# Kernel optimization log

Measured on AMD Instinct MI355X. Metric: run time of the kernel, lower is better.

Reference implementation:

```python
import jax, jax.numpy as jnp
import numpy as np

N_NODES = 50000
N_EDGES = 1600000
IN_FEAT = 128
HEADS = 8
OUT_FEAT = 16


def setup_inputs() -> dict:
    key = jax.random.key(0)
    ks = jax.random.split(key, 8)
    feat = jax.random.normal(ks[0], (N_NODES, IN_FEAT), dtype=jnp.float32)
    src = jax.random.randint(ks[1], (N_EDGES,), 0, N_NODES, dtype=jnp.int32)
    dst = jax.random.randint(ks[2], (N_EDGES,), 0, N_NODES, dtype=jnp.int32)
    eps = jax.random.normal(ks[3], (N_EDGES, HEADS), dtype=jnp.float32)
    # small init scale keeps exp(log_scale) numerically tame
    W_fc = jax.random.normal(ks[4], (IN_FEAT, HEADS * OUT_FEAT), dtype=jnp.float32) * 0.05
    W_post = jax.random.normal(ks[5], (OUT_FEAT, 4), dtype=jnp.float32) * 0.05
    b_post = jax.random.normal(ks[6], (4,), dtype=jnp.float32) * 0.05
    bias = jax.random.normal(ks[7], (HEADS, OUT_FEAT), dtype=jnp.float32) * 0.05
    return {"feat": feat, "src": src, "dst": dst, "eps": eps,
            "W_fc": W_fc, "W_post": W_post, "b_post": b_post, "bias": bias}


def reference(feat, src, dst, eps, W_fc, W_post, b_post, bias):
    N = feat.shape[0]
    # node projection: [N, H, F]
    h = (feat @ W_fc).reshape(N, HEADS, OUT_FEAT)
    # per-node posterior params: [N, H, 4] -> loc_l, loc_r, log_scale_l, log_scale_r
    post = jnp.einsum('nhf,fk->nhk', h, W_post) + b_post
    loc_l, loc_r, lsl, lsr = post[..., 0], post[..., 1], post[..., 2], post[..., 3]
    # per-edge score via reparameterized sample: [E, H]
    loc = loc_l[src] + loc_r[dst]
    log_scale = lsl[src] + lsr[dst]
    e = loc + jnp.exp(log_scale) * eps
    # edge softmax over incoming edges of each dst node (per head)
    m = jax.lax.stop_gradient(jax.ops.segment_max(e, dst, num_segments=N))
    ex = jnp.exp(e - m[dst])
    denom = jax.ops.segment_sum(ex, dst, num_segments=N)
    a = ex / denom[dst]
    # weighted aggregation: sum over in-edges of h[src] * a
    msg = h[src] * a[:, :, None]                     # [E, H, F]
    out = jax.ops.segment_sum(msg, dst, num_segments=N)  # [N, H, F]
    out = out + bias[None]
    return out
```

## Files before the change

### kernel.cpp

```cpp
#include <hip/hip_runtime.h>
#include <hip/hip_fp16.h>

#define IN_FEAT 128
#define HEADS 8
#define OUT_FEAT 16
#define HF 128
#define BSHIFT 6
#define BNODES 64
#define NBMAX 1024
#define CHUNK 4096
#define CAP 2560

__global__ __launch_bounds__(256) void init_kernel(int* __restrict__ bucket_cursor,
                                                   int nb)
{
    int i = blockIdx.x * 256 + threadIdx.x;
    if (i < nb) bucket_cursor[i] = i * CAP;
}

__device__ __forceinline__ void gemm_body(
    const float* __restrict__ feat, const float* __restrict__ W_fc,
    const float* __restrict__ W_post, const float* __restrict__ b_post,
    __half* __restrict__ hbuf, float2* __restrict__ postE,
    float2* __restrict__ postD, int N, int node_base, void* ldsraw)
{
    float4* lds4 = (float4*)ldsraw;
    float* lds = (float*)lds4;
    const int tid = threadIdx.x;

    const float4* f4 = (const float4*)feat;
    for (int i = tid; i < 32 * 32; i += 256) {
        int n = i >> 5, k4 = i & 31;
        int gn = node_base + n;
        float4 v = make_float4(0.f, 0.f, 0.f, 0.f);
        if (gn < N) v = f4[gn * 32 + k4];
        lds4[i] = v;
    }
    __syncthreads();

    const int cg = tid & 31, ng = tid >> 5;
    const int n0 = ng * 4;
    float acc[4][4];
#pragma unroll
    for (int i = 0; i < 4; i++) acc[i][0] = acc[i][1] = acc[i][2] = acc[i][3] = 0.f;

    const float4* W4 = (const float4*)W_fc;
#pragma unroll 4
    for (int k = 0; k < 128; ++k) {
        float4 w = W4[k * 32 + cg];
#pragma unroll
        for (int i = 0; i < 4; i++) {
            float f = lds[(n0 + i) * 128 + k];
            acc[i][0] += f * w.x; acc[i][1] += f * w.y;
            acc[i][2] += f * w.z; acc[i][3] += f * w.w;
        }
    }
    __half2* hb2 = (__half2*)hbuf;
#pragma unroll
    for (int i = 0; i < 4; i++) {
        int gn = node_base + n0 + i;
        if (gn < N) {
            union { uint2 u; __half2 h[2]; } pk;
            pk.h[0] = __floats2half2_rn(acc[i][0], acc[i][1]);
            pk.h[1] = __floats2half2_rn(acc[i][2], acc[i][3]);
            *(uint2*)&hb2[gn * 64 + cg * 2] = pk.u;
        }
    }
    __syncthreads();
#pragma unroll
    for (int i = 0; i < 4; i++)
        lds4[(n0 + i) * 32 + cg] = make_float4(acc[i][0], acc[i][1], acc[i][2], acc[i][3]);
    __syncthreads();

    {
        int n = tid >> 3, h = tid & 7;
        float p0 = b_post[0], p1 = b_post[1], p2 = b_post[2], p3 = b_post[3];
#pragma unroll
        for (int f = 0; f < 16; ++f) {
            float v = lds[n * 128 + h * 16 + f];
            p0 += v * W_post[f * 4 + 0];
            p1 += v * W_post[f * 4 + 1];
            p2 += v * W_post[f * 4 + 2];
            p3 += v * W_post[f * 4 + 3];
        }
        int gn = node_base + n;
        if (gn < N) {
            postE[gn * 8 + h] = make_float2(p0, p2);
            postD[gn * 8 + h] = make_float2(p1, p3);
        }
    }
}

__global__ __launch_bounds__(256) void gemm_scatter_kernel(
    const float* __restrict__ feat, const float* __restrict__ W_fc,
    const float* __restrict__ W_post, const float* __restrict__ b_post,
    __half* __restrict__ hbuf, float2* __restrict__ postE,
    float2* __restrict__ postD, int N,
    const int* __restrict__ src, const int* __restrict__ dst,
    int* __restrict__ bucket_cursor, uint2* __restrict__ recs, int E, int nb,
    int SB)
{
    __shared__ float4 lds4[32 * 32];
    const int tid = threadIdx.x;

    if (blockIdx.x < SB) {
        int* cnt  = (int*)lds4;
        int* base = cnt + NBMAX;
        for (int i = tid; i < nb; i += 256) cnt[i] = 0;
        __syncthreads();
        const int e0 = blockIdx.x * CHUNK;
        const int e1 = min(e0 + CHUNK, E);
        for (int e = e0 + tid; e < e1; e += 256)
            atomicAdd(&cnt[dst[e] >> BSHIFT], 1);
        __syncthreads();
        for (int i = tid; i < nb; i += 256) {
            int c = cnt[i];
            base[i] = c ? atomicAdd(&bucket_cursor[i], c) : 0;
            cnt[i] = 0;
        }
        __syncthreads();
        for (int e = e0 + tid; e < e1; e += 256) {
            int d = dst[e];
            int b = d >> BSHIFT;
            int slot = base[b] + atomicAdd(&cnt[b], 1);
            if (slot < (b + 1) * CAP)
                recs[slot] = make_uint2((unsigned)e,
                                        ((unsigned)src[e] << BSHIFT) | (unsigned)(d & (BNODES - 1)));
        }
        return;
    }

    gemm_body(feat, W_fc, W_post, b_post, hbuf, postE, postD, N,
              (int)(blockIdx.x - SB) * 32, (void*)lds4);
}

__global__ __launch_bounds__(256) void bucket_csr_kernel(
    const uint2* __restrict__ recs, const int* __restrict__ bucket_cursor,
    uint2* __restrict__ offs, uint2* __restrict__ csr, int N)
{
    __shared__ int ncnt[BNODES];
    __shared__ int snc[BNODES];
    const int b = blockIdx.x, tid = threadIdx.x;
    const int node_lo = b << BSHIFT;
    const int rlo = b * CAP;
    int rhi = bucket_cursor[b];
    if (rhi > rlo + CAP) rhi = rlo + CAP;
    const int gn = node_lo + tid;

    if (tid < BNODES) ncnt[tid] = 0;
    __syncthreads();
    for (int r = rlo + tid; r < rhi; r += 256)
        atomicAdd(&ncnt[recs[r].y & (BNODES - 1u)], 1);
    __syncthreads();
    if (tid < BNODES) snc[tid] = ncnt[tid];
    __syncthreads();
    for (int off = 1; off < BNODES; off <<= 1) {
        int t = (tid < BNODES && tid >= off) ? snc[tid - off] : 0;
        __syncthreads();
        if (tid < BNODES) snc[tid] += t;
        __syncthreads();
    }
    int cnt = (tid < BNODES) ? ncnt[tid] : 0;
    int excl = (tid < BNODES) ? snc[tid] - cnt : 0;
    if (tid < BNODES && gn < N) offs[gn] = make_uint2(rlo + excl, cnt);
    __syncthreads();
    if (tid < BNODES) ncnt[tid] = excl;
    __syncthreads();

    for (int r = rlo + tid; r < rhi; r += 256) {
        uint2 rec = recs[r];
        int dl = (int)(rec.y & (BNODES - 1u));
        unsigned s = rec.y >> BSHIFT;
        int slot = rlo + atomicAdd(&ncnt[dl], 1);
        csr[slot] = make_uint2(rec.x, s);
    }
}

__global__ __launch_bounds__(256) void agg_kernel(
    const uint2* __restrict__ csr, const uint2* __restrict__ offs,
    const float2* __restrict__ postE, const float2* __restrict__ postD,
    const float* __restrict__ eps,
    const __half* __restrict__ hbuf, const float* __restrict__ bias,
    float* __restrict__ out, int N)
{
    const int lane = threadIdx.x & 63;
    const int d = blockIdx.x * 4 + (threadIdx.x >> 6);
    if (d >= N) return;
    const uint2 od = offs[d];
    const int start = (int)od.x;
    const int deg = (int)od.y;
    const int j = lane >> 3, hh = lane & 7;
    const float2 dv = postD[(size_t)d * 8 + hh];

    float2 acc = make_float2(0.f, 0.f);
    float dsum = 0.f;

    int c = 0;
    for (; c + 8 <= deg; c += 8) {
        uint2 rec = csr[start + c + j];
        int e = (int)rec.x, s = (int)rec.y;
        float2 pv = postE[(size_t)s * 8 + hh];
        float ep = eps[(size_t)e * 8 + hh];
        float ex = __expf((pv.x + dv.x) + __expf(pv.y + dv.y) * ep);
#pragma unroll
        for (int jj = 0; jj < 8; ++jj) {
            float a = __shfl(ex, jj * 8 + j, 64);
            int  sj = __shfl(s, jj * 8, 64);
            float2 hv = __half22float2(((const __half2*)(hbuf + (size_t)sj * HF))[lane]);
            acc.x += a * hv.x;
            acc.y += a * hv.y;
            dsum += a;
        }
    }
    if (c < deg) {
        int jc = deg - c;
        uint2 rec = csr[start + c + min(j, jc - 1)];
        int e = (int)rec.x, s = (int)rec.y;
        float2 pv = postE[(size_t)s * 8 + hh];
        float ep = eps[(size_t)e * 8 + hh];
        float ex = (j < jc) ? __expf((pv.x + dv.x) + __expf(pv.y + dv.y) * ep) : 0.f;
        for (int jj = 0; jj < jc; ++jj) {
            float a = __shfl(ex, jj * 8 + j, 64);
            int  sj = __shfl(s, jj * 8, 64);
            float2 hv = __half22float2(((const __half2*)(hbuf + (size_t)sj * HF))[lane]);
            acc.x += a * hv.x;
            acc.y += a * hv.y;
            dsum += a;
        }
    }

    float inv = (dsum > 0.f) ? 1.f / dsum : 0.f;
    float2 bv = ((const float2*)bias)[lane];
    float2 o = make_float2(acc.x * inv + bv.x, acc.y * inv + bv.y);
    ((float2*)out)[(size_t)d * 64 + lane] = o;
}

extern "C" void kernel_launch(void* const* d_in, const int* in_sizes, int n_in,
                              void* d_out, int out_size, void* d_ws, size_t ws_size,
                              hipStream_t stream)
{
    const float* feat   = (const float*)d_in[0];
    const int*   src    = (const int*)d_in[1];
    const int*   dst    = (const int*)d_in[2];
    const float* eps    = (const float*)d_in[3];
    const float* W_fc   = (const float*)d_in[4];
    const float* W_post = (const float*)d_in[5];
    const float* b_post = (const float*)d_in[6];
    const float* bias   = (const float*)d_in[7];
    float* out = (float*)d_out;

    const int N = in_sizes[0] / IN_FEAT;
    const int E = in_sizes[1];
    const int nb = (N + BNODES - 1) >> BSHIFT;
    const int SB = (E + CHUNK - 1) / CHUNK;
    const int GB = (N + 31) / 32;

    char* p = (char*)d_ws;
    auto alloc = [&](size_t bytes) {
        char* r = p;
        p += (bytes + 255) & ~size_t(255);
        return r;
    };
    __half* hbuf    = (__half*)alloc((size_t)N * HF * 2);
    float2* postE   = (float2*)alloc((size_t)N * 8 * 8);
    float2* postD   = (float2*)alloc((size_t)N * 8 * 8);
    uint2*  offs    = (uint2*)alloc((size_t)N * 8);
    int*    bucket_cursor = (int*)alloc((size_t)(NBMAX + 1) * 4);
    uint2*  recs    = (uint2*)alloc((size_t)nb * CAP * 8);
    uint2*  csr     = (uint2*)alloc((size_t)nb * CAP * 8);

    init_kernel<<<(nb + 255) / 256, 256, 0, stream>>>(bucket_cursor, nb);
    gemm_scatter_kernel<<<SB + GB, 256, 0, stream>>>(
        feat, W_fc, W_post, b_post, hbuf, postE, postD, N,
        src, dst, bucket_cursor, recs, E, nb, SB);
    bucket_csr_kernel<<<nb, 256, 0, stream>>>(recs, bucket_cursor, offs, csr, N);
    agg_kernel<<<(N + 3) / 4, 256, 0, stream>>>(csr, offs, postE, postD, eps,
                                                hbuf, bias, out, N);
}
```

Measured before the change: 292.3 us.

## Pack eps to fp16 into bucket records and use 16-bit permutation instead of CSR copy

The scatter phase now reads each edge's eps row, converts it to half precision and stores it next to the bucketed record, so the aggregation reads eps from bucket-local memory rather than gathering randomly from the full fp32 eps array. The second pass writes only a 16-bit permutation index per edge instead of copying full CSR records. The aggregation kernel loads up to 64 permutation entries per wave and resolves src and eps through them. This trades random 32-byte eps gathers and a record copy for an extra indirection, half-precision eps (reduced accuracy), and larger scatter writes.

```diff
diff --git a/kernel.cpp b/kernel.cpp
--- a/kernel.cpp
+++ b/kernel.cpp
@@ -97,8 +97,9 @@
     __half* __restrict__ hbuf, float2* __restrict__ postE,
     float2* __restrict__ postD, int N,
     const int* __restrict__ src, const int* __restrict__ dst,
-    int* __restrict__ bucket_cursor, uint2* __restrict__ recs, int E, int nb,
-    int SB)
+    const float* __restrict__ eps,
+    int* __restrict__ bucket_cursor, unsigned* __restrict__ recsA,
+    uint4* __restrict__ recsE, int E, int nb, int SB)
 {
     __shared__ float4 lds4[32 * 32];
     const int tid = threadIdx.x;
@@ -119,13 +120,22 @@
             cnt[i] = 0;
         }
         __syncthreads();
+        const float4* e4 = (const float4*)eps;
         for (int e = e0 + tid; e < e1; e += 256) {
             int d = dst[e];
             int b = d >> BSHIFT;
             int slot = base[b] + atomicAdd(&cnt[b], 1);
-            if (slot < (b + 1) * CAP)
-                recs[slot] = make_uint2((unsigned)e,
-                                        ((unsigned)src[e] << BSHIFT) | (unsigned)(d & (BNODES - 1)));
+            if (slot < (b + 1) * CAP) {
+                float4 lo = e4[(size_t)e * 2];
+                float4 hi = e4[(size_t)e * 2 + 1];
+                union { uint4 u; __half2 h[4]; } pk;
+                pk.h[0] = __floats2half2_rn(lo.x, lo.y);
+                pk.h[1] = __floats2half2_rn(lo.z, lo.w);
+                pk.h[2] = __floats2half2_rn(hi.x, hi.y);
+                pk.h[3] = __floats2half2_rn(hi.z, hi.w);
+                recsA[slot] = ((unsigned)src[e] << BSHIFT) | (unsigned)(d & (BNODES - 1));
+                recsE[slot] = pk.u;
+            }
         }
         return;
     }
@@ -134,9 +144,9 @@
               (int)(blockIdx.x - SB) * 32, (void*)lds4);
 }
 
-__global__ __launch_bounds__(256) void bucket_csr_kernel(
-    const uint2* __restrict__ recs, const int* __restrict__ bucket_cursor,
-    uint2* __restrict__ offs, uint2* __restrict__ csr, int N)
+__global__ __launch_bounds__(256) void perm_kernel(
+    const unsigned* __restrict__ recsA, const int* __restrict__ bucket_cursor,
+    unsigned short* __restrict__ perm16, uint2* __restrict__ offs, int N)
 {
     __shared__ int ncnt[BNODES];
     __shared__ int snc[BNODES];
@@ -150,7 +160,7 @@
     if (tid < BNODES) ncnt[tid] = 0;
     __syncthreads();
     for (int r = rlo + tid; r < rhi; r += 256)
-        atomicAdd(&ncnt[recs[r].y & (BNODES - 1u)], 1);
+        atomicAdd(&ncnt[recsA[r] & (BNODES - 1u)], 1);
     __syncthreads();
     if (tid < BNODES) snc[tid] = ncnt[tid];
     __syncthreads();
@@ -168,18 +178,16 @@
     __syncthreads();
 
     for (int r = rlo + tid; r < rhi; r += 256) {
-        uint2 rec = recs[r];
-        int dl = (int)(rec.y & (BNODES - 1u));
-        unsigned s = rec.y >> BSHIFT;
-        int slot = rlo + atomicAdd(&ncnt[dl], 1);
-        csr[slot] = make_uint2(rec.x, s);
+        int dl = (int)(recsA[r] & (BNODES - 1u));
+        int q = atomicAdd(&ncnt[dl], 1);
+        perm16[rlo + q] = (unsigned short)(r - rlo);
     }
 }
 
 __global__ __launch_bounds__(256) void agg_kernel(
-    const uint2* __restrict__ csr, const uint2* __restrict__ offs,
+    const unsigned* __restrict__ recsA, const uint4* __restrict__ recsE,
+    const unsigned short* __restrict__ perm16, const uint2* __restrict__ offs,
     const float2* __restrict__ postE, const float2* __restrict__ postD,
-    const float* __restrict__ eps,
     const __half* __restrict__ hbuf, const float* __restrict__ bias,
     float* __restrict__ out, int N)
 {
@@ -189,44 +197,56 @@
     const uint2 od = offs[d];
     const int start = (int)od.x;
     const int deg = (int)od.y;
+    const int rbase = (d >> BSHIFT) * CAP;
     const int j = lane >> 3, hh = lane & 7;
     const float2 dv = postD[(size_t)d * 8 + hh];
+    const __half* epsH = (const __half*)recsE;
 
     float2 acc = make_float2(0.f, 0.f);
     float dsum = 0.f;
 
     int c = 0;
-    for (; c + 8 <= deg; c += 8) {
-        uint2 rec = csr[start + c + j];
-        int e = (int)rec.x, s = (int)rec.y;
-        float2 pv = postE[(size_t)s * 8 + hh];
-        float ep = eps[(size_t)e * 8 + hh];
-        float ex = __expf((pv.x + dv.x) + __expf(pv.y + dv.y) * ep);
-#pragma unroll
-        for (int jj = 0; jj < 8; ++jj) {
-            float a = __shfl(ex, jj * 8 + j, 64);
-            int  sj = __shfl(s, jj * 8, 64);
-            float2 hv = __half22float2(((const __half2*)(hbuf + (size_t)sj * HF))[lane]);
-            acc.x += a * hv.x;
-            acc.y += a * hv.y;
-            dsum += a;
-        }
-    }
-    if (c < deg) {
-        int jc = deg - c;
-        uint2 rec = csr[start + c + min(j, jc - 1)];
-        int e = (int)rec.x, s = (int)rec.y;
-        float2 pv = postE[(size_t)s * 8 + hh];
-        float ep = eps[(size_t)e * 8 + hh];
-        float ex = (j < jc) ? __expf((pv.x + dv.x) + __expf(pv.y + dv.y) * ep) : 0.f;
-        for (int jj = 0; jj < jc; ++jj) {
-            float a = __shfl(ex, jj * 8 + j, 64);
-            int  sj = __shfl(s, jj * 8, 64);
-            float2 hv = __half22float2(((const __half2*)(hbuf + (size_t)sj * HF))[lane]);
-            acc.x += a * hv.x;
-            acc.y += a * hv.y;
-            dsum += a;
-        }
+    while (c < deg) {
+        const int win = min(64, deg - c);
+        int li = c + ((lane < win) ? lane : (win - 1));
+        int p_all = (int)perm16[start + li];
+        int s_all = (int)(recsA[rbase + p_all] >> BSHIFT);
+
+        int cw = 0;
+        for (; cw + 8 <= win; cw += 8) {
+            int pj = __shfl(p_all, cw + j, 64);
+            int sj = __shfl(s_all, cw + j, 64);
+            float ep = __half2float(epsH[(size_t)(rbase + pj) * 8 + hh]);
+            float2 pv = postE[(size_t)sj * 8 + hh];
+            float ex = __expf((pv.x + dv.x) + __expf(pv.y + dv.y) * ep);
+#pragma unroll
+            for (int jj = 0; jj < 8; ++jj) {
+                float a = __shfl(ex, jj * 8 + j, 64);
+                int  sg = __shfl(s_all, cw + jj, 64);
+                float2 hv = __half22float2(((const __half2*)(hbuf + (size_t)sg * HF))[lane]);
+                acc.x += a * hv.x;
+                acc.y += a * hv.y;
+                dsum += a;
+            }
+        }
+        if (cw < win) {
+            int jc = win - cw;
+            int jj0 = cw + ((j < jc) ? j : (jc - 1));
+            int pj = __shfl(p_all, jj0, 64);
+            int sj = __shfl(s_all, jj0, 64);
+            float ep = __half2float(epsH[(size_t)(rbase + pj) * 8 + hh]);
+            float2 pv = postE[(size_t)sj * 8 + hh];
+            float ex = (j < jc) ? __expf((pv.x + dv.x) + __expf(pv.y + dv.y) * ep) : 0.f;
+            for (int jj = 0; jj < jc; ++jj) {
+                float a = __shfl(ex, jj * 8 + j, 64);
+                int  sg = __shfl(s_all, cw + jj, 64);
+                float2 hv = __half22float2(((const __half2*)(hbuf + (size_t)sg * HF))[lane]);
+                acc.x += a * hv.x;
+                acc.y += a * hv.y;
+                dsum += a;
+            }
+        }
+        c += win;
     }
 
     float inv = (dsum > 0.f) ? 1.f / dsum : 0.f;
@@ -266,14 +286,15 @@
     float2* postD   = (float2*)alloc((size_t)N * 8 * 8);
     uint2*  offs    = (uint2*)alloc((size_t)N * 8);
     int*    bucket_cursor = (int*)alloc((size_t)(NBMAX + 1) * 4);
-    uint2*  recs    = (uint2*)alloc((size_t)nb * CAP * 8);
-    uint2*  csr     = (uint2*)alloc((size_t)nb * CAP * 8);
+    unsigned*       recsA = (unsigned*)alloc((size_t)nb * CAP * 4);
+    uint4*          recsE = (uint4*)alloc((size_t)nb * CAP * 16);
+    unsigned short* perm16 = (unsigned short*)alloc((size_t)nb * CAP * 2);
 
     init_kernel<<<(nb + 255) / 256, 256, 0, stream>>>(bucket_cursor, nb);
     gemm_scatter_kernel<<<SB + GB, 256, 0, stream>>>(
         feat, W_fc, W_post, b_post, hbuf, postE, postD, N,
-        src, dst, bucket_cursor, recs, E, nb, SB);
-    bucket_csr_kernel<<<nb, 256, 0, stream>>>(recs, bucket_cursor, offs, csr, N);
-    agg_kernel<<<(N + 3) / 4, 256, 0, stream>>>(csr, offs, postE, postD, eps,
-                                                hbuf, bias, out, N);
-}
+        src, dst, eps, bucket_cursor, recsA, recsE, E, nb, SB);
+    perm_kernel<<<nb, 256, 0, stream>>>(recsA, bucket_cursor, perm16, offs, N);
+    agg_kernel<<<(N + 3) / 4, 256, 0, stream>>>(recsA, recsE, perm16, offs,
+                                                postE, postD, hbuf, bias, out, N);
+}
```

Result: slower. 323.7 us (+10.7%).

## Split node GEMM blocks between scatter and CSR-build kernels

Applied to the files above, without the earlier changes.

Moves part of the node projection GEMM blocks (beyond the first GA groups) out of the scatter kernel and into the bucket CSR-build kernel. The bucket blocks and the GEMM blocks now share one launch and a union of shared memory. The aim is to balance work across the two launches, so the CSR build, which has only about 782 blocks, no longer underfills the GPU while the scatter kernel carries all the GEMM work. The split point is a fixed constant, and the union raises the CSR blocks' LDS footprint, which may lower their occupancy.

```diff
diff --git a/kernel.cpp b/kernel.cpp
--- a/kernel.cpp
+++ b/kernel.cpp
@@ -10,6 +10,7 @@
 #define NBMAX 1024
 #define CHUNK 4096
 #define CAP 2560
+#define GA 1100
 
 __global__ __launch_bounds__(256) void init_kernel(int* __restrict__ bucket_cursor,
                                                    int nb)
@@ -134,46 +135,58 @@
               (int)(blockIdx.x - SB) * 32, (void*)lds4);
 }
 
-__global__ __launch_bounds__(256) void bucket_csr_kernel(
+__global__ __launch_bounds__(256) void csr_gemm_kernel(
     const uint2* __restrict__ recs, const int* __restrict__ bucket_cursor,
-    uint2* __restrict__ offs, uint2* __restrict__ csr, int N)
-{
-    __shared__ int ncnt[BNODES];
-    __shared__ int snc[BNODES];
-    const int b = blockIdx.x, tid = threadIdx.x;
-    const int node_lo = b << BSHIFT;
-    const int rlo = b * CAP;
-    int rhi = bucket_cursor[b];
-    if (rhi > rlo + CAP) rhi = rlo + CAP;
-    const int gn = node_lo + tid;
-
-    if (tid < BNODES) ncnt[tid] = 0;
-    __syncthreads();
-    for (int r = rlo + tid; r < rhi; r += 256)
-        atomicAdd(&ncnt[recs[r].y & (BNODES - 1u)], 1);
-    __syncthreads();
-    if (tid < BNODES) snc[tid] = ncnt[tid];
-    __syncthreads();
-    for (int off = 1; off < BNODES; off <<= 1) {
-        int t = (tid < BNODES && tid >= off) ? snc[tid - off] : 0;
-        __syncthreads();
-        if (tid < BNODES) snc[tid] += t;
-        __syncthreads();
-    }
-    int cnt = (tid < BNODES) ? ncnt[tid] : 0;
-    int excl = (tid < BNODES) ? snc[tid] - cnt : 0;
-    if (tid < BNODES && gn < N) offs[gn] = make_uint2(rlo + excl, cnt);
-    __syncthreads();
-    if (tid < BNODES) ncnt[tid] = excl;
-    __syncthreads();
-
-    for (int r = rlo + tid; r < rhi; r += 256) {
-        uint2 rec = recs[r];
-        int dl = (int)(rec.y & (BNODES - 1u));
-        unsigned s = rec.y >> BSHIFT;
-        int slot = rlo + atomicAdd(&ncnt[dl], 1);
-        csr[slot] = make_uint2(rec.x, s);
-    }
+    uint2* __restrict__ offs, uint2* __restrict__ csr, int N, int nb,
+    const float* __restrict__ feat, const float* __restrict__ W_fc,
+    const float* __restrict__ W_post, const float* __restrict__ b_post,
+    __half* __restrict__ hbuf, float2* __restrict__ postE,
+    float2* __restrict__ postD, int nbase0)
+{
+    __shared__ union { struct { int ncnt[BNODES]; int snc[BNODES]; } c;
+                       float4 g[32 * 32]; } u;
+    const int tid = threadIdx.x;
+
+    if (blockIdx.x < (unsigned)nb) {
+        const int b = blockIdx.x;
+        const int node_lo = b << BSHIFT;
+        const int rlo = b * CAP;
+        int rhi = bucket_cursor[b];
+        if (rhi > rlo + CAP) rhi = rlo + CAP;
+        const int gn = node_lo + tid;
+
+        if (tid < BNODES) u.c.ncnt[tid] = 0;
+        __syncthreads();
+        for (int r = rlo + tid; r < rhi; r += 256)
+            atomicAdd(&u.c.ncnt[recs[r].y & (BNODES - 1u)], 1);
+        __syncthreads();
+        if (tid < BNODES) u.c.snc[tid] = u.c.ncnt[tid];
+        __syncthreads();
+        for (int off = 1; off < BNODES; off <<= 1) {
+            int t = (tid < BNODES && tid >= off) ? u.c.snc[tid - off] : 0;
+            __syncthreads();
+            if (tid < BNODES) u.c.snc[tid] += t;
+            __syncthreads();
+        }
+        int cnt = (tid < BNODES) ? u.c.ncnt[tid] : 0;
+        int excl = (tid < BNODES) ? u.c.snc[tid] - cnt : 0;
+        if (tid < BNODES && gn < N) offs[gn] = make_uint2(rlo + excl, cnt);
+        __syncthreads();
+        if (tid < BNODES) u.c.ncnt[tid] = excl;
+        __syncthreads();
+
+        for (int r = rlo + tid; r < rhi; r += 256) {
+            uint2 rec = recs[r];
+            int dl = (int)(rec.y & (BNODES - 1u));
+            unsigned s = rec.y >> BSHIFT;
+            int slot = rlo + atomicAdd(&u.c.ncnt[dl], 1);
+            csr[slot] = make_uint2(rec.x, s);
+        }
+        return;
+    }
+
+    gemm_body(feat, W_fc, W_post, b_post, hbuf, postE, postD, N,
+              nbase0 + (int)(blockIdx.x - nb) * 32, (void*)u.g);
 }
 
 __global__ __launch_bounds__(256) void agg_kernel(
@@ -255,6 +268,9 @@
     const int SB = (E + CHUNK - 1) / CHUNK;
     const int GB = (N + 31) / 32;
 
+    int ga = GA; if (ga > GB) ga = GB;
+    int gbb = GB - ga;
+
     char* p = (char*)d_ws;
     auto alloc = [&](size_t bytes) {
         char* r = p;
@@ -270,10 +286,12 @@
     uint2*  csr     = (uint2*)alloc((size_t)nb * CAP * 8);
 
     init_kernel<<<(nb + 255) / 256, 256, 0, stream>>>(bucket_cursor, nb);
-    gemm_scatter_kernel<<<SB + GB, 256, 0, stream>>>(
+    gemm_scatter_kernel<<<SB + ga, 256, 0, stream>>>(
         feat, W_fc, W_post, b_post, hbuf, postE, postD, N,
         src, dst, bucket_cursor, recs, E, nb, SB);
-    bucket_csr_kernel<<<nb, 256, 0, stream>>>(recs, bucket_cursor, offs, csr, N);
+    csr_gemm_kernel<<<nb + gbb, 256, 0, stream>>>(
+        recs, bucket_cursor, offs, csr, N, nb,
+        feat, W_fc, W_post, b_post, hbuf, postE, postD, ga * 32);
     agg_kernel<<<(N + 3) / 4, 256, 0, stream>>>(csr, offs, postE, postD, eps,
                                                 hbuf, bias, out, N);
 }
```

After: 296.2 us. About the same (+1.4%).
